# Kernel tuning notes

Hardware: AMD Instinct MI355X
Metric: run time of the kernel (lower is better)

Reference implementation:

```python
import jax, jax.numpy as jnp
import numpy as np


def setup_inputs() -> dict:
    key = jax.random.key(0)
    x = jax.random.normal(key, (256, 64, 4096), dtype=jnp.float32)
    return {"x": x}


def _mat_shrinkage(cov, n):
    # cov: [B, p, p]; Rao-Blackwell Ledoit-Wolf shrinkage toward scaled identity
    p = cov.shape[-1]
    I = jnp.eye(p, dtype=cov.dtype)[None]                      # [1, p, p]
    trace = jnp.trace(cov, axis1=-2, axis2=-1)[:, None, None]  # [B, 1, 1]
    F_hat = trace / p * I                                      # [B, p, p]
    # tr(C @ C) without materializing C@C
    second_trace = jnp.einsum('bij,bji->b', cov, cov)[:, None, None]
    numerator = (n - 2) / n * second_trace + trace ** 2
    denominator = (n + 2) * (second_trace - trace ** 2 / p)
    rho = jnp.minimum(numerator / denominator, 1.0)
    return rho * F_hat + (1.0 - rho) * cov


def reference(x):
    # x: [B, C, M]
    B, C, M = x.shape
    x_mu = jnp.mean(x, axis=2, keepdims=True)          # [B, C, 1]
    x_cnt = x - x_mu                                    # [B, C, M]
    cov = jnp.einsum('bcm,bdm->bcd', x_cnt, x_cnt) / M  # [B, C, C]
    cov = _mat_shrinkage(cov, n=M)
    L = jnp.linalg.cholesky(jnp.linalg.inv(cov))        # [B, C, C], lower
    # Z = L^T @ x_cnt
    Z = jnp.einsum('bdc,bdm->bcm', L, x_cnt)            # [B, C, M]
    return Z
```

## Files before the change

kernel.cpp:

```cpp
#include <hip/hip_runtime.h>

#define B_ 256
#define C_ 64
#define M_ 4096
#define S_ 4
#define GSTRIDE 4160

typedef float f32x4_t __attribute__((ext_vector_type(4)));

__global__ __launch_bounds__(256, 4) void k_gram(const float* __restrict__ x,
                                                 float* __restrict__ wsA) {
    const int b = blockIdx.x;
    const int s = blockIdx.y;
    const int t = threadIdx.x;
    const int w = t >> 6;
    const int l = t & 63;

    __shared__ float St[2][64][68];
    __shared__ float ms[64][17];

    const float* xb = x + (size_t)b * (C_ * M_);
    float* g = wsA + (size_t)(b * S_ + s) * GSTRIDE;

    const int tc = l >> 3, td = l & 7;
    const int cl = l >> 2;
    const int m4 = l & 3;

    float acc[8][8];
#pragma unroll
    for (int i = 0; i < 8; ++i)
#pragma unroll
        for (int j = 0; j < 8; ++j) acc[i][j] = 0.f;
    float msum[4] = {0.f, 0.f, 0.f, 0.f};

    const int mbase = s * 1024 + w * 256;
    float4 r[4];
#pragma unroll
    for (int k = 0; k < 4; ++k)
        r[k] = *(const float4*)(xb + (size_t)(cl + 16 * k) * M_ + mbase + m4 * 4);

    for (int st = 0; st < 16; ++st) {
        const int p = st & 1;
#pragma unroll
        for (int k = 0; k < 4; ++k) {
            float4 v = r[k];
            msum[k] += v.x + v.y + v.z + v.w;
            const int row = w * 16 + m4 * 4;
            const int c = cl + 16 * k;
            St[p][row + 0][c] = v.x;
            St[p][row + 1][c] = v.y;
            St[p][row + 2][c] = v.z;
            St[p][row + 3][c] = v.w;
        }
        if (st < 15) {
#pragma unroll
            for (int k = 0; k < 4; ++k)
                r[k] = *(const float4*)(xb + (size_t)(cl + 16 * k) * M_ +
                                        mbase + (st + 1) * 16 + m4 * 4);
        }
        asm volatile("s_waitcnt lgkmcnt(0)" ::: "memory");
#pragma unroll 2
        for (int m = 0; m < 16; ++m) {
            float a[8], bb[8];
            *(float4*)&a[0]  = *(const float4*)&St[p][w * 16 + m][tc * 8];
            *(float4*)&a[4]  = *(const float4*)&St[p][w * 16 + m][tc * 8 + 4];
            *(float4*)&bb[0] = *(const float4*)&St[p][w * 16 + m][td * 8];
            *(float4*)&bb[4] = *(const float4*)&St[p][w * 16 + m][td * 8 + 4];
#pragma unroll
            for (int i = 0; i < 8; ++i)
#pragma unroll
                for (int j = 0; j < 8; ++j)
                    acc[i][j] = fmaf(a[i], bb[j], acc[i][j]);
        }
    }
#pragma unroll
    for (int k = 0; k < 4; ++k) ms[cl + 16 * k][w * 4 + m4] = msum[k];
    __syncthreads();

    if (w == 1) {
#pragma unroll
        for (int i = 0; i < 8; ++i) {
            *(float4*)&St[0][tc * 8 + i][td * 8]     = make_float4(acc[i][0], acc[i][1], acc[i][2], acc[i][3]);
            *(float4*)&St[0][tc * 8 + i][td * 8 + 4] = make_float4(acc[i][4], acc[i][5], acc[i][6], acc[i][7]);
        }
    } else if (w == 3) {
#pragma unroll
        for (int i = 0; i < 8; ++i) {
            *(float4*)&St[1][tc * 8 + i][td * 8]     = make_float4(acc[i][0], acc[i][1], acc[i][2], acc[i][3]);
            *(float4*)&St[1][tc * 8 + i][td * 8 + 4] = make_float4(acc[i][4], acc[i][5], acc[i][6], acc[i][7]);
        }
    }
    __syncthreads();
    if (w == 0) {
#pragma unroll
        for (int i = 0; i < 8; ++i) {
            float4 p = *(const float4*)&St[0][tc * 8 + i][td * 8];
            float4 q = *(const float4*)&St[0][tc * 8 + i][td * 8 + 4];
            acc[i][0] += p.x; acc[i][1] += p.y; acc[i][2] += p.z; acc[i][3] += p.w;
            acc[i][4] += q.x; acc[i][5] += q.y; acc[i][6] += q.z; acc[i][7] += q.w;
        }
    } else if (w == 2) {
#pragma unroll
        for (int i = 0; i < 8; ++i) {
            float4 p = *(const float4*)&St[1][tc * 8 + i][td * 8];
            float4 q = *(const float4*)&St[1][tc * 8 + i][td * 8 + 4];
            acc[i][0] += p.x; acc[i][1] += p.y; acc[i][2] += p.z; acc[i][3] += p.w;
            acc[i][4] += q.x; acc[i][5] += q.y; acc[i][6] += q.z; acc[i][7] += q.w;
        }
    }
    __syncthreads();
    if (w == 2) {
#pragma unroll
        for (int i = 0; i < 8; ++i) {
            *(float4*)&St[0][tc * 8 + i][td * 8]     = make_float4(acc[i][0], acc[i][1], acc[i][2], acc[i][3]);
            *(float4*)&St[0][tc * 8 + i][td * 8 + 4] = make_float4(acc[i][4], acc[i][5], acc[i][6], acc[i][7]);
        }
    }
    __syncthreads();
    if (w == 0) {
#pragma unroll
        for (int i = 0; i < 8; ++i) {
            float4 p = *(const float4*)&St[0][tc * 8 + i][td * 8];
            float4 q = *(const float4*)&St[0][tc * 8 + i][td * 8 + 4];
            float4 lo = make_float4(acc[i][0] + p.x, acc[i][1] + p.y,
                                    acc[i][2] + p.z, acc[i][3] + p.w);
            float4 hi = make_float4(acc[i][4] + q.x, acc[i][5] + q.y,
                                    acc[i][6] + q.z, acc[i][7] + q.w);
            *(float4*)(g + (size_t)(tc * 8 + i) * 64 + td * 8)     = lo;
            *(float4*)(g + (size_t)(tc * 8 + i) * 64 + td * 8 + 4) = hi;
        }
    } else if (w == 1) {
        float sum = 0.f;
#pragma unroll
        for (int q = 0; q < 16; ++q) sum += ms[l][q];
        g[4096 + l] = sum;
    }
}

__global__ __launch_bounds__(256) void k_chol(const float* __restrict__ wsA,
                                              float* __restrict__ wsB) {
    const int b = blockIdx.x;
    const int t = threadIdx.x;

    __shared__ float Cw[64][68];
    __shared__ float Ww[64][68];
    __shared__ float mu[64];
    __shared__ float red[256];
    __shared__ float ucol[64];
    __shared__ float sc[4];

    const float* pa = wsA + (size_t)b * S_ * GSTRIDE;
    float* o = wsB + (size_t)b * GSTRIDE;

    for (int idx = t; idx < 4096; idx += 256) {
        float v = 0.f;
#pragma unroll
        for (int s = 0; s < S_; ++s) v += pa[(size_t)s * GSTRIDE + idx];
        Cw[idx >> 6][idx & 63] = v;
    }
    if (t < 64) {
        float v = 0.f;
#pragma unroll
        for (int s = 0; s < S_; ++s) v += pa[(size_t)s * GSTRIDE + 4096 + t];
        mu[t] = v * (1.0f / M_);
    }
    __syncthreads();
    for (int idx = t; idx < 4096; idx += 256) {
        int i = idx >> 6, j = idx & 63;
        Cw[i][j] = Cw[i][j] * (1.0f / M_) - mu[i] * mu[j];
    }
    __syncthreads();

    {
        float trp = 0.f, stp = 0.f;
        for (int idx = t; idx < 4096; idx += 256) {
            int i = idx >> 6, j = idx & 63;
            float v = Cw[i][j];
            stp = fmaf(v, Cw[j][i], stp);
            if (i == j) trp += v;
        }
        red[t] = stp;
        __syncthreads();
        for (int off = 128; off > 0; off >>= 1) {
            if (t < off) red[t] += red[t + off];
            __syncthreads();
        }
        if (t == 0) sc[1] = red[0];
        __syncthreads();
        red[t] = trp;
        __syncthreads();
        for (int off = 128; off > 0; off >>= 1) {
            if (t < off) red[t] += red[t + off];
            __syncthreads();
        }
        if (t == 0) {
            float tr = red[0], st = sc[1];
            const float n = (float)M_, p = 64.f;
            float num = (n - 2.f) / n * st + tr * tr;
            float den = (n + 2.f) * (st - tr * tr / p);
            float rho = fminf(num / den, 1.0f);
            sc[0] = tr;
            sc[2] = rho;
        }
        __syncthreads();
        float rho = sc[2], tr = sc[0];
        float dadd = rho * tr * (1.0f / 64.0f);
        for (int idx = t; idx < 4096; idx += 256) {
            int i = idx >> 6, j = idx & 63;
            float v = (1.f - rho) * Cw[i][j];
            if (i == j) v += dadd;
            Cw[i][j] = v;
        }
    }

    for (int k = 63; k >= 0; --k) {
        __syncthreads();
        float dkk = sqrtf(Cw[k][k]);
        float dinv = 1.0f / dkk;
        for (int i = t; i < k; i += 256) ucol[i] = Cw[i][k] * dinv;
        if (t == 0) ucol[k] = dkk;
        __syncthreads();
        const int nel = (k * (k + 1)) >> 1;
        for (int e = t; e < nel; e += 256) {
            int j = (int)((sqrtf((float)(8 * e + 1)) - 1.0f) * 0.5f);
            if (e < ((j * (j + 1)) >> 1)) --j;
            else if (e >= (((j + 1) * (j + 2)) >> 1)) ++j;
            int i = e - ((j * (j + 1)) >> 1);
            Cw[i][j] = fmaf(-ucol[i], ucol[j], Cw[i][j]);
        }
        for (int i = t; i <= k; i += 256) Cw[i][k] = ucol[i];
    }
    __syncthreads();

    if (t < 64) {
        const int j = t;
        Ww[j][j] = 1.0f / Cw[j][j];
        for (int i = j - 1; i >= 0; --i) {
            float s0 = 0.f, s1 = 0.f;
            int lq = i + 1;
            for (; lq + 1 <= j; lq += 2) {
                s0 = fmaf(Cw[i][lq], Ww[lq][j], s0);
                s1 = fmaf(Cw[i][lq + 1], Ww[lq + 1][j], s1);
            }
            if (lq <= j) s0 = fmaf(Cw[i][lq], Ww[lq][j], s0);
            Ww[i][j] = -(s0 + s1) / Cw[i][i];
        }
    }
    __syncthreads();
    if (t < 64) {
        float s = 0.f;
        for (int d = t; d < 64; ++d) s = fmaf(Ww[t][d], mu[d], s);
        o[4096 + t] = s;
    }
    for (int idx = t; idx < 4096; idx += 256) {
        int d = idx >> 6, c = idx & 63;
        o[idx] = (d >= c) ? Ww[c][d] : 0.f;
    }
}

__global__ __launch_bounds__(256, 4) void k_apply(const float* __restrict__ x,
                                                  const float* __restrict__ wsB,
                                                  float* __restrict__ out) {
    const int b = blockIdx.x;
    const int s = blockIdx.y;
    const int t = threadIdx.x;
    const int w = t >> 6;

    __shared__ float Wt[64][68];
    __shared__ float St[64][68];
    __shared__ float wmu[64];

    const float* xb = x + (size_t)b * (C_ * M_);
    float* ob = out + (size_t)b * (C_ * M_);
    const float* wsb = wsB + (size_t)b * GSTRIDE;

    for (int idx = t; idx < 4096; idx += 256) Wt[idx >> 6][idx & 63] = wsb[idx];
    if (t < 64) wmu[t] = wsb[4096 + t];

    const int tc5 = t >> 4;
    const int tm5 = t & 15;
    const int cld = t >> 4;
    const int m45 = t & 15;
    const int d0 = w * 16;
    const int mbase = s * 1024;

    float4 r2[4];
#pragma unroll
    for (int k = 0; k < 4; ++k)
        r2[k] = *(const float4*)(xb + (size_t)(cld + 16 * k) * M_ + mbase + m45 * 4);

    for (int ch = 0; ch < 16; ++ch) {
        const int m0 = mbase + ch * 64;
        __syncthreads();
#pragma unroll
        for (int k = 0; k < 4; ++k)
            *(float4*)&St[cld + 16 * k][m45 * 4] = r2[k];
        if (ch < 15) {
#pragma unroll
            for (int k = 0; k < 4; ++k)
                r2[k] = *(const float4*)(xb + (size_t)(cld + 16 * k) * M_ +
                                         m0 + 64 + m45 * 4);
        }
        __syncthreads();
        float a2[4][4];
#pragma unroll
        for (int i = 0; i < 4; ++i)
#pragma unroll
            for (int j = 0; j < 4; ++j) a2[i][j] = 0.f;
#pragma unroll 2
        for (int d = d0; d < 64; ++d) {
            float4 a  = *(const float4*)&Wt[d][tc5 * 4];
            float4 bv = *(const float4*)&St[d][tm5 * 4];
            a2[0][0] = fmaf(a.x, bv.x, a2[0][0]);
            a2[0][1] = fmaf(a.x, bv.y, a2[0][1]);
            a2[0][2] = fmaf(a.x, bv.z, a2[0][2]);
            a2[0][3] = fmaf(a.x, bv.w, a2[0][3]);
            a2[1][0] = fmaf(a.y, bv.x, a2[1][0]);
            a2[1][1] = fmaf(a.y, bv.y, a2[1][1]);
            a2[1][2] = fmaf(a.y, bv.z, a2[1][2]);
            a2[1][3] = fmaf(a.y, bv.w, a2[1][3]);
            a2[2][0] = fmaf(a.z, bv.x, a2[2][0]);
            a2[2][1] = fmaf(a.z, bv.y, a2[2][1]);
            a2[2][2] = fmaf(a.z, bv.z, a2[2][2]);
            a2[2][3] = fmaf(a.z, bv.w, a2[2][3]);
            a2[3][0] = fmaf(a.w, bv.x, a2[3][0]);
            a2[3][1] = fmaf(a.w, bv.y, a2[3][1]);
            a2[3][2] = fmaf(a.w, bv.z, a2[3][2]);
            a2[3][3] = fmaf(a.w, bv.w, a2[3][3]);
        }
#pragma unroll
        for (int i = 0; i < 4; ++i) {
            const int c = tc5 * 4 + i;
            float wv = wmu[c];
            f32x4_t ov = {a2[i][0] - wv, a2[i][1] - wv,
                          a2[i][2] - wv, a2[i][3] - wv};
            __builtin_nontemporal_store(
                ov, (f32x4_t*)(ob + (size_t)c * M_ + m0 + tm5 * 4));
        }
    }
}

__global__ __launch_bounds__(256) void k_fused(const float* __restrict__ x,
                                               float* __restrict__ out) {
    const int b = blockIdx.x;
    const int t = threadIdx.x;
    const int w = t >> 6;
    const int l = t & 63;

    __shared__ float St[64][68];
    __shared__ float Cw[64][68];
    __shared__ float Ww[64][68];
    __shared__ float ms[64][17];
    __shared__ float mu[64];
    __shared__ float red[256];
    __shared__ float ucol[64];
    __shared__ float wmu[64];
    __shared__ float sc[4];

    const float* xb = x + (size_t)b * (C_ * M_);
    float* ob = out + (size_t)b * (C_ * M_);

    const int tc = l >> 3, td = l & 7;
    const int cl = l >> 2;
    const int m4 = l & 3;

    float acc[8][8];
#pragma unroll
    for (int i = 0; i < 8; ++i)
#pragma unroll
        for (int j = 0; j < 8; ++j) acc[i][j] = 0.f;
    float msum[4] = {0.f, 0.f, 0.f, 0.f};

    const int mbase = w * 1024;
    float4 r[4];
#pragma unroll
    for (int k = 0; k < 4; ++k)
        r[k] = *(const float4*)(xb + (size_t)(cl + 16 * k) * M_ + mbase + m4 * 4);

    for (int s = 0; s < 64; ++s) {
        __syncthreads();
#pragma unroll
        for (int k = 0; k < 4; ++k) {
            float4 v = r[k];
            msum[k] += v.x + v.y + v.z + v.w;
            const int row = w * 16 + m4 * 4;
            const int c = cl + 16 * k;
            St[row + 0][c] = v.x;
            St[row + 1][c] = v.y;
            St[row + 2][c] = v.z;
            St[row + 3][c] = v.w;
        }
        if (s < 63) {
#pragma unroll
            for (int k = 0; k < 4; ++k)
                r[k] = *(const float4*)(xb + (size_t)(cl + 16 * k) * M_ +
                                        mbase + (s + 1) * 16 + m4 * 4);
        }
        __syncthreads();
#pragma unroll 2
        for (int m = 0; m < 16; ++m) {
            float a[8], bb[8];
            *(float4*)&a[0]  = *(const float4*)&St[w * 16 + m][tc * 8];
            *(float4*)&a[4]  = *(const float4*)&St[w * 16 + m][tc * 8 + 4];
            *(float4*)&bb[0] = *(const float4*)&St[w * 16 + m][td * 8];
            *(float4*)&bb[4] = *(const float4*)&St[w * 16 + m][td * 8 + 4];
#pragma unroll
            for (int i = 0; i < 8; ++i)
#pragma unroll
                for (int j = 0; j < 8; ++j)
                    acc[i][j] = fmaf(a[i], bb[j], acc[i][j]);
        }
    }
#pragma unroll
    for (int k = 0; k < 4; ++k) ms[cl + 16 * k][w * 4 + m4] = msum[k];
    __syncthreads();

    if (w == 1) {
#pragma unroll
        for (int i = 0; i < 8; ++i) {
            *(float4*)&Ww[tc * 8 + i][td * 8]     = make_float4(acc[i][0], acc[i][1], acc[i][2], acc[i][3]);
            *(float4*)&Ww[tc * 8 + i][td * 8 + 4] = make_float4(acc[i][4], acc[i][5], acc[i][6], acc[i][7]);
        }
        float s = 0.f;
#pragma unroll
        for (int q = 0; q < 16; ++q) s += ms[l][q];
        mu[l] = s * (1.0f / M_);
    } else if (w == 2) {
#pragma unroll
        for (int i = 0; i < 8; ++i) {
            *(float4*)&Cw[tc * 8 + i][td * 8]     = make_float4(acc[i][0], acc[i][1], acc[i][2], acc[i][3]);
            *(float4*)&Cw[tc * 8 + i][td * 8 + 4] = make_float4(acc[i][4], acc[i][5], acc[i][6], acc[i][7]);
        }
    } else if (w == 3) {
#pragma unroll
        for (int i = 0; i < 8; ++i) {
            *(float4*)&St[tc * 8 + i][td * 8]     = make_float4(acc[i][0], acc[i][1], acc[i][2], acc[i][3]);
            *(float4*)&St[tc * 8 + i][td * 8 + 4] = make_float4(acc[i][4], acc[i][5], acc[i][6], acc[i][7]);
        }
    }
    __syncthreads();
    if (w == 0) {
#pragma unroll
        for (int i = 0; i < 8; ++i) {
            float4 p0 = *(const float4*)&Ww[tc * 8 + i][td * 8];
            float4 p1 = *(const float4*)&Cw[tc * 8 + i][td * 8];
            float4 p2 = *(const float4*)&St[tc * 8 + i][td * 8];
            float4 q0 = *(const float4*)&Ww[tc * 8 + i][td * 8 + 4];
            float4 q1 = *(const float4*)&Cw[tc * 8 + i][td * 8 + 4];
            float4 q2 = *(const float4*)&St[tc * 8 + i][td * 8 + 4];
            float4 lo = make_float4(acc[i][0] + p0.x + p1.x + p2.x,
                                    acc[i][1] + p0.y + p1.y + p2.y,
                                    acc[i][2] + p0.z + p1.z + p2.z,
                                    acc[i][3] + p0.w + p1.w + p2.w);
            float4 hi = make_float4(acc[i][4] + q0.x + q1.x + q2.x,
                                    acc[i][5] + q0.y + q1.y + q2.y,
                                    acc[i][6] + q0.z + q1.z + q2.z,
                                    acc[i][7] + q0.w + q1.w + q2.w);
            *(float4*)&Cw[tc * 8 + i][td * 8]     = lo;
            *(float4*)&Cw[tc * 8 + i][td * 8 + 4] = hi;
        }
    }
    __syncthreads();
    for (int idx = t; idx < 4096; idx += 256) {
        int i = idx >> 6, j = idx & 63;
        Cw[i][j] = Cw[i][j] * (1.0f / M_) - mu[i] * mu[j];
    }
    __syncthreads();

    {
        float trp = 0.f, stp = 0.f;
        for (int idx = t; idx < 4096; idx += 256) {
            int i = idx >> 6, j = idx & 63;
            float v = Cw[i][j];
            stp = fmaf(v, Cw[j][i], stp);
            if (i == j) trp += v;
        }
        red[t] = stp;
        __syncthreads();
        for (int off = 128; off > 0; off >>= 1) {
            if (t < off) red[t] += red[t + off];
            __syncthreads();
        }
        if (t == 0) sc[1] = red[0];
        __syncthreads();
        red[t] = trp;
        __syncthreads();
        for (int off = 128; off > 0; off >>= 1) {
            if (t < off) red[t] += red[t + off];
            __syncthreads();
        }
        if (t == 0) {
            float tr = red[0], st = sc[1];
            const float n = (float)M_, p = 64.f;
            float num = (n - 2.f) / n * st + tr * tr;
            float den = (n + 2.f) * (st - tr * tr / p);
            float rho = fminf(num / den, 1.0f);
            sc[0] = tr;
            sc[2] = rho;
        }
        __syncthreads();
        float rho = sc[2], tr = sc[0];
        float dadd = rho * tr * (1.0f / 64.0f);
        for (int idx = t; idx < 4096; idx += 256) {
            int i = idx >> 6, j = idx & 63;
            float v = (1.f - rho) * Cw[i][j];
            if (i == j) v += dadd;
            Cw[i][j] = v;
        }
    }

    for (int k = 63; k >= 0; --k) {
        __syncthreads();
        float dkk = sqrtf(Cw[k][k]);
        float dinv = 1.0f / dkk;
        for (int i = t; i < k; i += 256) ucol[i] = Cw[i][k] * dinv;
        if (t == 0) ucol[k] = dkk;
        __syncthreads();
        const int nel = (k * (k + 1)) >> 1;
        for (int e = t; e < nel; e += 256) {
            int j = (int)((sqrtf((float)(8 * e + 1)) - 1.0f) * 0.5f);
            if (e < ((j * (j + 1)) >> 1)) --j;
            else if (e >= (((j + 1) * (j + 2)) >> 1)) ++j;
            int i = e - ((j * (j + 1)) >> 1);
            Cw[i][j] = fmaf(-ucol[i], ucol[j], Cw[i][j]);
        }
        for (int i = t; i <= k; i += 256) Cw[i][k] = ucol[i];
    }
    __syncthreads();

    if (t < 64) {
        const int j = t;
        Ww[j][j] = 1.0f / Cw[j][j];
        for (int i = j - 1; i >= 0; --i) {
            float s0 = 0.f, s1 = 0.f;
            int lq = i + 1;
            for (; lq + 1 <= j; lq += 2) {
                s0 = fmaf(Cw[i][lq], Ww[lq][j], s0);
                s1 = fmaf(Cw[i][lq + 1], Ww[lq + 1][j], s1);
            }
            if (lq <= j) s0 = fmaf(Cw[i][lq], Ww[lq][j], s0);
            Ww[i][j] = -(s0 + s1) / Cw[i][i];
        }
    }
    __syncthreads();
    if (t < 64) {
        float s = 0.f;
        for (int d = t; d < 64; ++d) s = fmaf(Ww[t][d], mu[d], s);
        wmu[t] = s;
    }
    for (int idx = t; idx < 4096; idx += 256) {
        int d = idx >> 6, c = idx & 63;
        Cw[d][c] = (d >= c) ? Ww[c][d] : 0.f;
    }

    const int tc5 = t >> 5;
    const int tm5 = t & 31;
    const int cld = t >> 4;
    const int m45 = t & 15;
    const int d0 = w * 16;

    float4 r2[4];
#pragma unroll
    for (int k = 0; k < 4; ++k)
        r2[k] = *(const float4*)(xb + (size_t)(cld + 16 * k) * M_ + m45 * 4);

    for (int ch = 0; ch < 64; ++ch) {
        const int m0 = ch * 64;
        __syncthreads();
#pragma unroll
        for (int k = 0; k < 4; ++k)
            *(float4*)&St[cld + 16 * k][m45 * 4] = r2[k];
        if (ch < 63) {
#pragma unroll
            for (int k = 0; k < 4; ++k)
                r2[k] = *(const float4*)(xb + (size_t)(cld + 16 * k) * M_ +
                                         m0 + 64 + m45 * 4);
        }
        __syncthreads();
        float a2[8][2];
#pragma unroll
        for (int i = 0; i < 8; ++i) a2[i][0] = a2[i][1] = 0.f;
        for (int d = d0; d < 64; ++d) {
            float a[8];
            *(float4*)&a[0] = *(const float4*)&Cw[d][tc5 * 8];
            *(float4*)&a[4] = *(const float4*)&Cw[d][tc5 * 8 + 4];
            float2 bv = *(const float2*)&St[d][tm5 * 2];
#pragma unroll
            for (int i = 0; i < 8; ++i) {
                a2[i][0] = fmaf(a[i], bv.x, a2[i][0]);
                a2[i][1] = fmaf(a[i], bv.y, a2[i][1]);
            }
        }
#pragma unroll
        for (int i = 0; i < 8; ++i) {
            const int c = tc5 * 8 + i;
            float wv = wmu[c];
            float2 o = make_float2(a2[i][0] - wv, a2[i][1] - wv);
            *(float2*)(ob + (size_t)c * M_ + m0 + tm5 * 2) = o;
        }
    }
}

extern "C" void kernel_launch(void* const* d_in, const int* in_sizes, int n_in,
                              void* d_out, int out_size, void* d_ws, size_t ws_size,
                              hipStream_t stream) {
    const float* x = (const float*)d_in[0];
    float* out = (float*)d_out;
    const size_t needed = (size_t)(B_ * S_ + B_) * GSTRIDE * sizeof(float);
    if (d_ws && ws_size >= needed) {
        float* wsA = (float*)d_ws;
        float* wsB = wsA + (size_t)B_ * S_ * GSTRIDE;
        k_gram<<<dim3(B_, S_), 256, 0, stream>>>(x, wsA);
        k_chol<<<dim3(B_), 256, 0, stream>>>(wsA, wsB);
        k_apply<<<dim3(B_, S_), 256, 0, stream>>>(x, wsB, out);
    } else {
        k_fused<<<dim3(B_), 256, 0, stream>>>(x, out);
    }
}
```

Before: 749.4 us.

## Read x directly from global in k_apply and double the grid split

The apply kernel drops its shared-memory staging tile and register prefetch. Each thread now loads its float4 of x straight from global memory inside the reduction loop, which relies on L1/L2 to serve the reuse across the 16 thread rows. Removing the tile frees LDS and removes two barriers per chunk, so occupancy is raised to 8 blocks and the M dimension is split into 8 slices instead of 4. Nontemporal stores are replaced with plain stores. The risks are redundant global/cache traffic and exposed load latency in place of LDS reads.

New measurement: 844.1 us. 12.6% more time.

```diff
diff --git a/kernel.cpp b/kernel.cpp
--- a/kernel.cpp
+++ b/kernel.cpp
@@ -4,9 +4,8 @@
 #define C_ 64
 #define M_ 4096
 #define S_ 4
+#define AS_ 8
 #define GSTRIDE 4160
-
-typedef float f32x4_t __attribute__((ext_vector_type(4)));
 
 __global__ __launch_bounds__(256, 4) void k_gram(const float* __restrict__ x,
                                                  float* __restrict__ wsA) {
@@ -258,7 +257,7 @@
     }
 }
 
-__global__ __launch_bounds__(256, 4) void k_apply(const float* __restrict__ x,
+__global__ __launch_bounds__(256, 8) void k_apply(const float* __restrict__ x,
                                                   const float* __restrict__ wsB,
                                                   float* __restrict__ out) {
     const int b = blockIdx.x;
@@ -267,7 +266,6 @@
     const int w = t >> 6;
 
     __shared__ float Wt[64][68];
-    __shared__ float St[64][68];
     __shared__ float wmu[64];
 
     const float* xb = x + (size_t)b * (C_ * M_);
@@ -276,41 +274,26 @@
 
     for (int idx = t; idx < 4096; idx += 256) Wt[idx >> 6][idx & 63] = wsb[idx];
     if (t < 64) wmu[t] = wsb[4096 + t];
+    __syncthreads();
 
     const int tc5 = t >> 4;
     const int tm5 = t & 15;
-    const int cld = t >> 4;
-    const int m45 = t & 15;
     const int d0 = w * 16;
-    const int mbase = s * 1024;
-
-    float4 r2[4];
-#pragma unroll
-    for (int k = 0; k < 4; ++k)
-        r2[k] = *(const float4*)(xb + (size_t)(cld + 16 * k) * M_ + mbase + m45 * 4);
-
-    for (int ch = 0; ch < 16; ++ch) {
+    const int mbase = s * (M_ / AS_);
+
+    for (int ch = 0; ch < (M_ / AS_) / 64; ++ch) {
         const int m0 = mbase + ch * 64;
-        __syncthreads();
-#pragma unroll
-        for (int k = 0; k < 4; ++k)
-            *(float4*)&St[cld + 16 * k][m45 * 4] = r2[k];
-        if (ch < 15) {
-#pragma unroll
-            for (int k = 0; k < 4; ++k)
-                r2[k] = *(const float4*)(xb + (size_t)(cld + 16 * k) * M_ +
-                                         m0 + 64 + m45 * 4);
-        }
-        __syncthreads();
         float a2[4][4];
 #pragma unroll
         for (int i = 0; i < 4; ++i)
 #pragma unroll
             for (int j = 0; j < 4; ++j) a2[i][j] = 0.f;
-#pragma unroll 2
-        for (int d = d0; d < 64; ++d) {
+
+        const float* xp = xb + (size_t)d0 * M_ + m0 + tm5 * 4;
+#pragma unroll 4
+        for (int d = d0; d < 64; ++d, xp += M_) {
+            float4 bv = *(const float4*)xp;
             float4 a  = *(const float4*)&Wt[d][tc5 * 4];
-            float4 bv = *(const float4*)&St[d][tm5 * 4];
             a2[0][0] = fmaf(a.x, bv.x, a2[0][0]);
             a2[0][1] = fmaf(a.x, bv.y, a2[0][1]);
             a2[0][2] = fmaf(a.x, bv.z, a2[0][2]);
@@ -332,10 +315,9 @@
         for (int i = 0; i < 4; ++i) {
             const int c = tc5 * 4 + i;
             float wv = wmu[c];
-            f32x4_t ov = {a2[i][0] - wv, a2[i][1] - wv,
-                          a2[i][2] - wv, a2[i][3] - wv};
-            __builtin_nontemporal_store(
-                ov, (f32x4_t*)(ob + (size_t)c * M_ + m0 + tm5 * 4));
+            float4 o = make_float4(a2[i][0] - wv, a2[i][1] - wv,
+                                   a2[i][2] - wv, a2[i][3] - wv);
+            *(float4*)(ob + (size_t)c * M_ + m0 + tm5 * 4) = o;
         }
     }
 }
@@ -612,7 +594,7 @@
         float* wsB = wsA + (size_t)B_ * S_ * GSTRIDE;
         k_gram<<<dim3(B_, S_), 256, 0, stream>>>(x, wsA);
         k_chol<<<dim3(B_), 256, 0, stream>>>(wsA, wsB);
-        k_apply<<<dim3(B_, S_), 256, 0, stream>>>(x, wsB, out);
+        k_apply<<<dim3(B_, AS_), 256, 0, stream>>>(x, wsB, out);
     } else {
         k_fused<<<dim3(B_), 256, 0, stream>>>(x, out);
     }
```
